# Kernel optimization log

Hardware: AMD Instinct MI355X
Metric: run time of the kernel (lower is better)

## Reference

```python
import jax, jax.numpy as jnp
import numpy as np

B, T, DQ, DV, A, F, K = 64, 1024, 1024, 512, 512, 32, 31


def setup_inputs() -> dict:
    key = jax.random.key(0)
    ks = jax.random.split(key, 8)
    query = jax.random.normal(ks[0], (B, DQ), jnp.float32)
    values = jax.random.normal(ks[1], (B, T, DV), jnp.float32)
    # decoder-step states (as produced by init_states)
    attention_cum = jnp.zeros((B, T), jnp.float32)
    attention_old = jnp.zeros((B, T), jnp.float32)
    alpha = jnp.concatenate([jnp.ones((B, 1), jnp.float32),
                             jnp.zeros((B, T - 1), jnp.float32) + 1e-7], axis=1)
    # learned parameters (Glorot-ish scaling)
    W_query = jax.random.normal(ks[2], (DQ, A), jnp.float32) / np.sqrt(DQ)
    W_inputs = jax.random.normal(ks[3], (DV, A), jnp.float32) / np.sqrt(DV)
    v_w = jax.random.normal(ks[4], (A, 1), jnp.float32) / np.sqrt(A)
    v_b = jnp.zeros((1,), jnp.float32)
    loc_kernel = jax.random.normal(ks[5], (K, 2, F), jnp.float32) / np.sqrt(K * 2)  # WIO
    W_loc = jax.random.normal(ks[6], (F, A), jnp.float32) / np.sqrt(F)
    return {"query": query, "values": values, "attention_cum": attention_cum,
            "attention_old": attention_old, "alpha": alpha,
            "W_query": W_query, "W_inputs": W_inputs, "v_w": v_w, "v_b": v_b,
            "loc_kernel": loc_kernel, "W_loc": W_loc}


def reference(query, values, attention_cum, attention_old, alpha,
              W_query, W_inputs, v_w, v_b, loc_kernel, W_loc):
    # process_values: cached projection of encoder memory  [B,T,A]
    processed_values = jnp.einsum('btd,da->bta', values, W_inputs)
    # location features: conv over stacked (old, cum) attention  [B,T,2]->[B,T,F]
    attn_cat = jnp.stack([attention_old, attention_cum], axis=2)
    conv = jax.lax.conv_general_dilated(attn_cat, loc_kernel, window_strides=(1,),
                                        padding='SAME',
                                        dimension_numbers=('NWC', 'WIO', 'NWC'))
    processed_attn = jnp.einsum('btf,fa->bta', conv, W_loc)
    # query projection  [B,1,A]
    processed_query = (query @ W_query)[:, None, :]
    # additive score  [B,T]
    score = (jnp.tanh(processed_values + processed_query + processed_attn) @ v_w)[..., 0] + v_b
    scores_norm = jax.nn.softmax(score, axis=-1)
    # forward attention recursion
    fwd_shifted = jnp.pad(alpha[:, :-1], ((0, 0), (1, 0)))
    new_alpha = (0.5 * alpha + 0.5 * fwd_shifted + 1e-8) * scores_norm
    new_alpha = new_alpha / jnp.sum(new_alpha, axis=1, keepdims=True)
    attn_weights = new_alpha
    # updated states
    new_cum = attention_cum + scores_norm
    new_old = attn_weights
    # context vector  [B,DV]
    context = jnp.einsum('bt,btd->bd', attn_weights, values)
    return (context, attn_weights, new_cum, new_old, new_alpha)
```

## Files before the change

kernel.cpp:

```cpp
#include <hip/hip_runtime.h>
#include <hip/hip_bf16.h>
#include <cstdint>
#include <cstddef>

#define B 64
#define T 1024
#define DQ 1024
#define DV 512
#define A_DIM 512
#define F_DIM 32
#define KW 31
#define M_TOT (B*T)
#define KEXT 544
#define NCHUNK 17

typedef __attribute__((ext_vector_type(8))) short short8;
typedef __attribute__((ext_vector_type(4))) float f32x4;

static __device__ __forceinline__ unsigned short f2bf(float f) {
    unsigned int u = __builtin_bit_cast(unsigned int, f);
    u += 0x7fffu + ((u >> 16) & 1u);
    return (unsigned short)(u >> 16);
}

static __device__ __forceinline__ float tanh_fast(float x) {
    float e = __expf(2.0f * x);
    return 1.0f - 2.0f * __builtin_amdgcn_rcpf(e + 1.0f);
}

__global__ void pq_kernel(const float* __restrict__ query, const float* __restrict__ Wq,
                          float* __restrict__ pq) {
    __shared__ float red[4][64];
    int b = blockIdx.x >> 3, a0 = (blockIdx.x & 7) * 64;
    int al = threadIdx.x & 63, ks = threadIdx.x >> 6;
    const float* qr = query + (size_t)b * DQ + ks * 256;
    const float* wc = Wq + (size_t)(ks * 256) * A_DIM + a0 + al;
    float acc = 0.f;
    #pragma unroll 8
    for (int k = 0; k < 256; ++k) acc += qr[k] * wc[(size_t)k * A_DIM];
    red[ks][al] = acc;
    __syncthreads();
    if (ks == 0) {
        float s = red[0][al] + red[1][al] + red[2][al] + red[3][al];
        pq[b * A_DIM + a0 + al] = s;
    }
}

__global__ void bt_kernel(const float* __restrict__ Wi, const float* __restrict__ Wl,
                          unsigned short* __restrict__ Bt) {
    int a = blockIdx.x;
    for (int k = threadIdx.x; k < KEXT; k += 256) {
        float v = (k < DV) ? Wi[(size_t)k * A_DIM + a] : Wl[(size_t)(k - DV) * A_DIM + a];
        Bt[(size_t)a * KEXT + k] = f2bf(v);
    }
}

__global__ void conv_kernel(const float* __restrict__ old_, const float* __restrict__ cum_,
                            const float* __restrict__ lk, unsigned short* __restrict__ convb) {
    __shared__ float sOld[158], sCum[158];
    __shared__ float sLK[KW * 2 * F_DIM];
    int b = blockIdx.x >> 3, t0 = (blockIdx.x & 7) * 128;
    int tid = threadIdx.x;
    for (int j = tid; j < 158; j += 128) {
        int tt = t0 - 15 + j;
        bool ok = (tt >= 0 && tt < T);
        sOld[j] = ok ? old_[b * T + tt] : 0.f;
        sCum[j] = ok ? cum_[b * T + tt] : 0.f;
    }
    for (int j = tid; j < KW * 2 * F_DIM; j += 128) sLK[j] = lk[j];
    __syncthreads();
    float acc[F_DIM];
    #pragma unroll
    for (int f = 0; f < F_DIM; ++f) acc[f] = 0.f;
    for (int k = 0; k < KW; ++k) {
        float o = sOld[tid + k], c = sCum[tid + k];
        const float* lo = &sLK[(k * 2 + 0) * F_DIM];
        const float* lc = &sLK[(k * 2 + 1) * F_DIM];
        #pragma unroll
        for (int f = 0; f < F_DIM; ++f) acc[f] += o * lo[f] + c * lc[f];
    }
    unsigned short* dst = convb + (size_t)(b * T + t0 + tid) * F_DIM;
    #pragma unroll
    for (int f = 0; f < F_DIM; ++f) dst[f] = f2bf(acc[f]);
}

__launch_bounds__(256, 2)
__global__ void gemm_score(const float* __restrict__ values,
                           const unsigned short* __restrict__ Bt,
                           const unsigned short* __restrict__ convb,
                           const float* __restrict__ pq,
                           const float* __restrict__ vw,
                           float* __restrict__ score) {
    __shared__ __align__(16) short sA[64 * 40];
    __shared__ __align__(16) short sB[512 * 40];
    __shared__ float sPQ[512];
    __shared__ float sVW[512];
    __shared__ float sSc[64];
    int tid = threadIdx.x;
    int m0 = blockIdx.x * 64;
    int b = m0 >> 10;
    for (int j = tid; j < 512; j += 256) { sPQ[j] = pq[b * 512 + j]; sVW[j] = vw[j]; }
    int w = tid >> 6, lane = tid & 63, q = lane >> 4, l15 = lane & 15;
    int wm = w & 1, wn = w >> 1;
    f32x4 acc0[16], acc1[16];
    #pragma unroll
    for (int n = 0; n < 16; ++n) { acc0[n] = (f32x4)0.f; acc1[n] = (f32x4)0.f; }
    int arow = tid >> 2, aseg = tid & 3;
    for (int c = 0; c < NCHUNK; ++c) {
        __syncthreads();
        if (c < 16) {
            const float* src = values + (size_t)(m0 + arow) * DV + c * 32 + aseg * 8;
            float4 x0 = *(const float4*)src;
            float4 x1 = *(const float4*)(src + 4);
            short8 pk;
            pk[0] = (short)f2bf(x0.x); pk[1] = (short)f2bf(x0.y);
            pk[2] = (short)f2bf(x0.z); pk[3] = (short)f2bf(x0.w);
            pk[4] = (short)f2bf(x1.x); pk[5] = (short)f2bf(x1.y);
            pk[6] = (short)f2bf(x1.z); pk[7] = (short)f2bf(x1.w);
            *(short8*)&sA[arow * 40 + aseg * 8] = pk;
        } else {
            short8 pk = *(const short8*)(const void*)(convb + (size_t)(m0 + arow) * F_DIM + aseg * 8);
            *(short8*)&sA[arow * 40 + aseg * 8] = pk;
        }
        #pragma unroll
        for (int j = 0; j < 8; ++j) {
            int task = j * 256 + tid;
            int a = task >> 2, seg = task & 3;
            short8 pk = *(const short8*)(const void*)(Bt + (size_t)a * KEXT + c * 32 + seg * 8);
            *(short8*)&sB[a * 40 + seg * 8] = pk;
        }
        __syncthreads();
        short8 af0 = *(const short8*)&sA[(wm * 32 + l15) * 40 + q * 8];
        short8 af1 = *(const short8*)&sA[(wm * 32 + 16 + l15) * 40 + q * 8];
        #pragma unroll
        for (int n = 0; n < 16; ++n) {
            short8 bfr = *(const short8*)&sB[(wn * 256 + n * 16 + l15) * 40 + q * 8];
            acc0[n] = __builtin_amdgcn_mfma_f32_16x16x32_bf16(af0, bfr, acc0[n], 0, 0, 0);
            acc1[n] = __builtin_amdgcn_mfma_f32_16x16x32_bf16(af1, bfr, acc1[n], 0, 0, 0);
        }
    }
    float prt[2][4];
    #pragma unroll
    for (int mb = 0; mb < 2; ++mb) {
        #pragma unroll
        for (int r = 0; r < 4; ++r) {
            float s = 0.f;
            #pragma unroll
            for (int n = 0; n < 16; ++n) {
                int col = wn * 256 + n * 16 + l15;
                float x = (mb ? acc1[n][r] : acc0[n][r]) + sPQ[col];
                s += tanh_fast(x) * sVW[col];
            }
            #pragma unroll
            for (int off = 1; off < 16; off <<= 1) s += __shfl_xor(s, off, 64);
            prt[mb][r] = s;
        }
    }
    if (wn == 0 && l15 == 0) {
        #pragma unroll
        for (int mb = 0; mb < 2; ++mb)
            #pragma unroll
            for (int r = 0; r < 4; ++r)
                sSc[wm * 32 + mb * 16 + q * 4 + r] = prt[mb][r];
    }
    __syncthreads();
    if (wn == 1 && l15 == 0) {
        #pragma unroll
        for (int mb = 0; mb < 2; ++mb)
            #pragma unroll
            for (int r = 0; r < 4; ++r) {
                int row = wm * 32 + mb * 16 + q * 4 + r;
                score[m0 + row] = sSc[row] + prt[mb][r];
            }
    }
}

__global__ void softmax_fwd(const float* __restrict__ score,
                            const float* __restrict__ alpha,
                            const float* __restrict__ cum,
                            float* __restrict__ out) {
    int b = blockIdx.x, t = threadIdx.x;
    __shared__ float sred[16];
    __shared__ float sbc;
    float sc = score[b * T + t];
    int wid = t >> 6, lane = t & 63;
    float m = sc;
    #pragma unroll
    for (int off = 32; off; off >>= 1) m = fmaxf(m, __shfl_xor(m, off, 64));
    if (lane == 0) sred[wid] = m;
    __syncthreads();
    if (t == 0) { float mm = sred[0]; for (int i = 1; i < 16; ++i) mm = fmaxf(mm, sred[i]); sbc = mm; }
    __syncthreads();
    float M = sbc;
    float e = __expf(sc - M);
    float s = e;
    #pragma unroll
    for (int off = 32; off; off >>= 1) s += __shfl_xor(s, off, 64);
    __syncthreads();
    if (lane == 0) sred[wid] = s;
    __syncthreads();
    if (t == 0) { float ss = 0.f; for (int i = 0; i < 16; ++i) ss += sred[i]; sbc = ss; }
    __syncthreads();
    float sn = e / sbc;
    float a_t = alpha[b * T + t];
    float a_p = (t > 0) ? alpha[b * T + t - 1] : 0.f;
    float ua = (0.5f * (a_t + a_p) + 1e-8f) * sn;
    float u = ua;
    #pragma unroll
    for (int off = 32; off; off >>= 1) u += __shfl_xor(u, off, 64);
    __syncthreads();
    if (lane == 0) sred[wid] = u;
    __syncthreads();
    if (t == 0) { float ss = 0.f; for (int i = 0; i < 16; ++i) ss += sred[i]; sbc = ss; }
    __syncthreads();
    float wgt = ua / sbc;
    float* attnw  = out + B * DV;
    float* ncum   = attnw + B * T;
    float* nold   = ncum + B * T;
    float* nalpha = nold + B * T;
    attnw[b * T + t]  = wgt;
    ncum[b * T + t]   = cum[b * T + t] + sn;
    nold[b * T + t]   = wgt;
    nalpha[b * T + t] = wgt;
    if (t < DV) out[b * DV + t] = 0.f;
}

__global__ void context_kernel(const float* __restrict__ values, float* __restrict__ out) {
    const float* attnw = out + B * DV;
    int bid = blockIdx.x;
    int b = bid >> 4, r = bid & 15, dh = r & 1, sl = r >> 1;
    int d = dh * 256 + threadIdx.x;
    float acc = 0.f;
    int tbase = sl * 128;
    #pragma unroll 4
    for (int tt = 0; tt < 128; ++tt) {
        int t = tbase + tt;
        acc += attnw[b * T + t] * values[(size_t)(b * T + t) * DV + d];
    }
    atomicAdd(&out[b * DV + d], acc);
}

extern "C" void kernel_launch(void* const* d_in, const int* in_sizes, int n_in,
                              void* d_out, int out_size, void* d_ws, size_t ws_size,
                              hipStream_t stream) {
    const float* query  = (const float*)d_in[0];
    const float* values = (const float*)d_in[1];
    const float* cum    = (const float*)d_in[2];
    const float* old_   = (const float*)d_in[3];
    const float* alpha  = (const float*)d_in[4];
    const float* Wq     = (const float*)d_in[5];
    const float* Wi     = (const float*)d_in[6];
    const float* vw     = (const float*)d_in[7];
    const float* lk     = (const float*)d_in[9];
    const float* Wl     = (const float*)d_in[10];
    float* out = (float*)d_out;
    char* ws = (char*)d_ws;
    float* ws_pq            = (float*)(ws);
    float* ws_score         = (float*)(ws + 131072);
    unsigned short* ws_Bt   = (unsigned short*)(ws + 393216);
    unsigned short* ws_conv = (unsigned short*)(ws + 1048576);

    pq_kernel<<<512, 256, 0, stream>>>(query, Wq, ws_pq);
    bt_kernel<<<512, 256, 0, stream>>>(Wi, Wl, ws_Bt);
    conv_kernel<<<512, 128, 0, stream>>>(old_, cum, lk, ws_conv);
    gemm_score<<<1024, 256, 0, stream>>>(values, ws_Bt, ws_conv, ws_pq, vw, ws_score);
    softmax_fwd<<<64, 1024, 0, stream>>>(ws_score, alpha, cum, out);
    context_kernel<<<1024, 256, 0, stream>>>(values, out);
}
```

Before: 314.9 us.

## Retile score GEMM to 128x256 with 32x32 MFMA and atomic score reduction

The score GEMM now gives each block a 128-row by 256-column tile, splitting the 512-wide attention dimension across two blocks, and uses 32x32x16 bf16 MFMA instructions instead of 16x16x32. Partial scores from the two column halves and from the two warp groups are combined with atomicAdd into a score buffer that pq_kernel now zeroes. This aims to cut per-block B-matrix loading and raise MFMA efficiency, but values rows are converted twice (once per column half) and atomics are added. The context kernel is also split into twice as many blocks, each covering half as many timesteps, to expose more parallelism.

Result: faster. 307.9 us (-2.2%).

```diff
diff --git a/kernel.cpp b/kernel.cpp
--- a/kernel.cpp
+++ b/kernel.cpp
@@ -16,6 +16,7 @@
 
 typedef __attribute__((ext_vector_type(8))) short short8;
 typedef __attribute__((ext_vector_type(4))) float f32x4;
+typedef __attribute__((ext_vector_type(16))) float f32x16;
 
 static __device__ __forceinline__ unsigned short f2bf(float f) {
     unsigned int u = __builtin_bit_cast(unsigned int, f);
@@ -29,8 +30,10 @@
 }
 
 __global__ void pq_kernel(const float* __restrict__ query, const float* __restrict__ Wq,
-                          float* __restrict__ pq) {
+                          float* __restrict__ pq, float* __restrict__ score) {
     __shared__ float red[4][64];
+    int gid = blockIdx.x * 256 + threadIdx.x;
+    if (gid < M_TOT) score[gid] = 0.f;
     int b = blockIdx.x >> 3, a0 = (blockIdx.x & 7) * 64;
     int al = threadIdx.x & 63, ks = threadIdx.x >> 6;
     const float* qr = query + (size_t)b * DQ + ks * 256;
@@ -91,87 +94,89 @@
                            const float* __restrict__ pq,
                            const float* __restrict__ vw,
                            float* __restrict__ score) {
-    __shared__ __align__(16) short sA[64 * 40];
-    __shared__ __align__(16) short sB[512 * 40];
-    __shared__ float sPQ[512];
-    __shared__ float sVW[512];
-    __shared__ float sSc[64];
+    __shared__ __align__(16) short sA[128 * 40];
+    __shared__ __align__(16) short sB[256 * 40];
+    __shared__ float sPQ[256];
+    __shared__ float sVW[256];
     int tid = threadIdx.x;
-    int m0 = blockIdx.x * 64;
+    int mt = blockIdx.x >> 1, ch = blockIdx.x & 1;
+    int m0 = mt * 128, n0 = ch * 256;
     int b = m0 >> 10;
-    for (int j = tid; j < 512; j += 256) { sPQ[j] = pq[b * 512 + j]; sVW[j] = vw[j]; }
-    int w = tid >> 6, lane = tid & 63, q = lane >> 4, l15 = lane & 15;
+    for (int j = tid; j < 256; j += 256) {
+        sPQ[j] = pq[b * A_DIM + n0 + j];
+        sVW[j] = vw[n0 + j];
+    }
+    int w = tid >> 6, lane = tid & 63;
+    int l31 = lane & 31, lh = lane >> 5;
     int wm = w & 1, wn = w >> 1;
-    f32x4 acc0[16], acc1[16];
-    #pragma unroll
-    for (int n = 0; n < 16; ++n) { acc0[n] = (f32x4)0.f; acc1[n] = (f32x4)0.f; }
-    int arow = tid >> 2, aseg = tid & 3;
+    f32x16 acc[2][4];
+    #pragma unroll
+    for (int mi = 0; mi < 2; ++mi)
+        #pragma unroll
+        for (int ni = 0; ni < 4; ++ni) acc[mi][ni] = (f32x16)0.f;
+
     for (int c = 0; c < NCHUNK; ++c) {
         __syncthreads();
-        if (c < 16) {
-            const float* src = values + (size_t)(m0 + arow) * DV + c * 32 + aseg * 8;
-            float4 x0 = *(const float4*)src;
-            float4 x1 = *(const float4*)(src + 4);
+        #pragma unroll
+        for (int j = 0; j < 2; ++j) {
+            int task = j * 256 + tid;
+            int row = task >> 2, seg = task & 3;
             short8 pk;
-            pk[0] = (short)f2bf(x0.x); pk[1] = (short)f2bf(x0.y);
-            pk[2] = (short)f2bf(x0.z); pk[3] = (short)f2bf(x0.w);
-            pk[4] = (short)f2bf(x1.x); pk[5] = (short)f2bf(x1.y);
-            pk[6] = (short)f2bf(x1.z); pk[7] = (short)f2bf(x1.w);
-            *(short8*)&sA[arow * 40 + aseg * 8] = pk;
-        } else {
-            short8 pk = *(const short8*)(const void*)(convb + (size_t)(m0 + arow) * F_DIM + aseg * 8);
-            *(short8*)&sA[arow * 40 + aseg * 8] = pk;
-        }
-        #pragma unroll
-        for (int j = 0; j < 8; ++j) {
+            if (c < 16) {
+                const float* src = values + (size_t)(m0 + row) * DV + c * 32 + seg * 8;
+                float4 x0 = *(const float4*)src;
+                float4 x1 = *(const float4*)(src + 4);
+                pk[0] = (short)f2bf(x0.x); pk[1] = (short)f2bf(x0.y);
+                pk[2] = (short)f2bf(x0.z); pk[3] = (short)f2bf(x0.w);
+                pk[4] = (short)f2bf(x1.x); pk[5] = (short)f2bf(x1.y);
+                pk[6] = (short)f2bf(x1.z); pk[7] = (short)f2bf(x1.w);
+            } else {
+                pk = *(const short8*)(const void*)(convb + (size_t)(m0 + row) * F_DIM + seg * 8);
+            }
+            *(short8*)&sA[row * 40 + seg * 8] = pk;
+        }
+        #pragma unroll
+        for (int j = 0; j < 4; ++j) {
             int task = j * 256 + tid;
-            int a = task >> 2, seg = task & 3;
-            short8 pk = *(const short8*)(const void*)(Bt + (size_t)a * KEXT + c * 32 + seg * 8);
-            *(short8*)&sB[a * 40 + seg * 8] = pk;
+            int ar = task >> 2, seg = task & 3;
+            short8 pk = *(const short8*)(const void*)(Bt + (size_t)(n0 + ar) * KEXT + c * 32 + seg * 8);
+            *(short8*)&sB[ar * 40 + seg * 8] = pk;
         }
         __syncthreads();
-        short8 af0 = *(const short8*)&sA[(wm * 32 + l15) * 40 + q * 8];
-        short8 af1 = *(const short8*)&sA[(wm * 32 + 16 + l15) * 40 + q * 8];
-        #pragma unroll
-        for (int n = 0; n < 16; ++n) {
-            short8 bfr = *(const short8*)&sB[(wn * 256 + n * 16 + l15) * 40 + q * 8];
-            acc0[n] = __builtin_amdgcn_mfma_f32_16x16x32_bf16(af0, bfr, acc0[n], 0, 0, 0);
-            acc1[n] = __builtin_amdgcn_mfma_f32_16x16x32_bf16(af1, bfr, acc1[n], 0, 0, 0);
-        }
-    }
-    float prt[2][4];
-    #pragma unroll
-    for (int mb = 0; mb < 2; ++mb) {
-        #pragma unroll
-        for (int r = 0; r < 4; ++r) {
+        #pragma unroll
+        for (int kk = 0; kk < 2; ++kk) {
+            short8 af[2], bf[4];
+            #pragma unroll
+            for (int mi = 0; mi < 2; ++mi)
+                af[mi] = *(const short8*)&sA[(wm * 64 + mi * 32 + l31) * 40 + kk * 16 + lh * 8];
+            #pragma unroll
+            for (int ni = 0; ni < 4; ++ni)
+                bf[ni] = *(const short8*)&sB[(wn * 128 + ni * 32 + l31) * 40 + kk * 16 + lh * 8];
+            #pragma unroll
+            for (int mi = 0; mi < 2; ++mi)
+                #pragma unroll
+                for (int ni = 0; ni < 4; ++ni)
+                    acc[mi][ni] = __builtin_amdgcn_mfma_f32_32x32x16_bf16(af[mi], bf[ni], acc[mi][ni], 0, 0, 0);
+        }
+    }
+    #pragma unroll
+    for (int mi = 0; mi < 2; ++mi) {
+        #pragma unroll
+        for (int r = 0; r < 16; ++r) {
             float s = 0.f;
             #pragma unroll
-            for (int n = 0; n < 16; ++n) {
-                int col = wn * 256 + n * 16 + l15;
-                float x = (mb ? acc1[n][r] : acc0[n][r]) + sPQ[col];
-                s += tanh_fast(x) * sVW[col];
+            for (int ni = 0; ni < 4; ++ni) {
+                int bcol = wn * 128 + ni * 32 + l31;
+                float x = acc[mi][ni][r] + sPQ[bcol];
+                s += tanh_fast(x) * sVW[bcol];
             }
             #pragma unroll
-            for (int off = 1; off < 16; off <<= 1) s += __shfl_xor(s, off, 64);
-            prt[mb][r] = s;
-        }
-    }
-    if (wn == 0 && l15 == 0) {
-        #pragma unroll
-        for (int mb = 0; mb < 2; ++mb)
-            #pragma unroll
-            for (int r = 0; r < 4; ++r)
-                sSc[wm * 32 + mb * 16 + q * 4 + r] = prt[mb][r];
-    }
-    __syncthreads();
-    if (wn == 1 && l15 == 0) {
-        #pragma unroll
-        for (int mb = 0; mb < 2; ++mb)
-            #pragma unroll
-            for (int r = 0; r < 4; ++r) {
-                int row = wm * 32 + mb * 16 + q * 4 + r;
-                score[m0 + row] = sSc[row] + prt[mb][r];
+            for (int off = 1; off < 32; off <<= 1) s += __shfl_xor(s, off, 64);
+            if (l31 == 0) {
+                int row = wm * 64 + mi * 32 + (r & 3) + 8 * (r >> 2) + 4 * lh;
+                atomicAdd(&score[m0 + row], s);
             }
+        }
     }
 }
 
@@ -228,12 +233,12 @@
 __global__ void context_kernel(const float* __restrict__ values, float* __restrict__ out) {
     const float* attnw = out + B * DV;
     int bid = blockIdx.x;
-    int b = bid >> 4, r = bid & 15, dh = r & 1, sl = r >> 1;
+    int b = bid >> 5, r = bid & 31, dh = r & 1, sl = r >> 1;
     int d = dh * 256 + threadIdx.x;
     float acc = 0.f;
-    int tbase = sl * 128;
+    int tbase = sl * 64;
     #pragma unroll 4
-    for (int tt = 0; tt < 128; ++tt) {
+    for (int tt = 0; tt < 64; ++tt) {
         int t = tbase + tt;
         acc += attnw[b * T + t] * values[(size_t)(b * T + t) * DV + d];
     }
@@ -260,10 +265,10 @@
     unsigned short* ws_Bt   = (unsigned short*)(ws + 393216);
     unsigned short* ws_conv = (unsigned short*)(ws + 1048576);
 
-    pq_kernel<<<512, 256, 0, stream>>>(query, Wq, ws_pq);
+    pq_kernel<<<512, 256, 0, stream>>>(query, Wq, ws_pq, ws_score);
     bt_kernel<<<512, 256, 0, stream>>>(Wi, Wl, ws_Bt);
     conv_kernel<<<512, 128, 0, stream>>>(old_, cum, lk, ws_conv);
     gemm_score<<<1024, 256, 0, stream>>>(values, ws_Bt, ws_conv, ws_pq, vw, ws_score);
     softmax_fwd<<<64, 1024, 0, stream>>>(ws_score, alpha, cum, out);
-    context_kernel<<<1024, 256, 0, stream>>>(values, out);
-}
+    context_kernel<<<2048, 256, 0, stream>>>(values, out);
+}
```
